# Performance work log

Measured on AMD Instinct MI355X. Metric: run time of the kernel, lower is better.

The kernel has to match this reference:

```python
import jax, jax.numpy as jnp
import numpy as np

N, E, C, L = 50000, 625000, 128, 4
H = 2 * C  # hidden size of per-layer ObjectModel
FRAC_SCALE = 1.0 / 16.0   # fractional_bitwidth = 4
Q_MAX = 8.0               # int_bitwidth = 4 -> signed fixed point range [-8, 8 - 1/16]


def fq(x):
    """Fixed-point fake-quantize (4 int bits, 4 frac bits, signed)."""
    return jnp.clip(jnp.round(x / FRAC_SCALE) * FRAC_SCALE, -Q_MAX, Q_MAX - FRAC_SCALE)


def qlin(h, W, b):
    # QuantLinear: input/weight/bias/output all quantized
    return fq(fq(h) @ fq(W) + fq(b))


def qbn(h, w, b):
    # BatchNorm1dToQuantScaleBias in inference: per-channel scale + bias
    return fq(fq(h) * fq(w) + fq(b))


def setup_inputs() -> dict:
    key = jax.random.key(0)
    ks = jax.random.split(key, 24)
    d = {}
    d["x"] = jax.random.normal(ks[0], (N, 3), dtype=jnp.float32)
    d["edge_attr"] = jax.random.normal(ks[1], (E, 4), dtype=jnp.float32)
    d["edge_index"] = jax.random.randint(ks[2], (2, E), 0, N, dtype=jnp.int64)
    # encoders
    d["node_W"] = jax.random.normal(ks[3], (3, C), dtype=jnp.float32) * 0.4
    d["node_b"] = jax.random.normal(ks[4], (C,), dtype=jnp.float32) * 0.2
    d["edge_W"] = jax.random.normal(ks[5], (4, C), dtype=jnp.float32) * 0.4
    d["edge_b"] = jax.random.normal(ks[6], (C,), dtype=jnp.float32) * 0.2
    d["node_bn_w"] = 1.0 + 0.1 * jax.random.normal(ks[7], (C,), dtype=jnp.float32)
    d["node_bn_b"] = 0.1 * jax.random.normal(ks[8], (C,), dtype=jnp.float32)
    d["edge_bn_w"] = 1.0 + 0.1 * jax.random.normal(ks[9], (C,), dtype=jnp.float32)
    d["edge_bn_b"] = 0.1 * jax.random.normal(ks[10], (C,), dtype=jnp.float32)
    # per-layer ObjectModel params (stacked over L)
    d["W1"] = jax.random.normal(ks[11], (L, C, H), dtype=jnp.float32) * (0.5 / np.sqrt(C))
    d["b1"] = jax.random.normal(ks[12], (L, H), dtype=jnp.float32) * 0.1
    d["bn_w"] = 1.0 + 0.1 * jax.random.normal(ks[13], (L, H), dtype=jnp.float32)
    d["bn_b"] = 0.1 * jax.random.normal(ks[14], (L, H), dtype=jnp.float32)
    d["W2"] = jax.random.normal(ks[15], (L, H, C), dtype=jnp.float32) * (0.5 / np.sqrt(H))
    d["b2"] = jax.random.normal(ks[16], (L, C), dtype=jnp.float32) * 0.1
    d["fc_W"] = jax.random.normal(ks[17], (C, 1), dtype=jnp.float32) * (0.5 / np.sqrt(C))
    d["fc_b"] = jax.random.normal(ks[18], (1,), dtype=jnp.float32) * 0.1
    return d


def reference(x, edge_attr, edge_index, node_W, node_b, edge_W, edge_b,
              node_bn_w, node_bn_b, edge_bn_w, edge_bn_b,
              W1, b1, bn_w, bn_b, W2, b2, fc_W, fc_b):
    src = edge_index[0]  # x_j (source) under flow='source_to_target'
    tgt = edge_index[1]  # aggregation target i

    h = fq(qlin(x, node_W, node_b))            # node encoder [N, C]
    e = fq(qlin(edge_attr, edge_W, edge_b))    # edge encoder [E, C]
    h = qbn(h, node_bn_w, node_bn_b)
    e = qbn(e, edge_bn_w, edge_bn_b)

    for l in range(L):
        # message: quant(x_j) + quant(edge_attr), QuantReLU
        msg = fq(jax.nn.relu(fq(h[src]) + fq(e)))          # [E, C]
        agg = jax.ops.segment_sum(msg, tgt, num_segments=N)  # scatter-sum [N, C]
        u = fq(agg)
        # ObjectModel: QuantLinear -> ScaleBias BN -> QuantReLU -> QuantLinear, then QuantIdentity
        z = qlin(u, W1[l], b1[l])
        z = qbn(z, bn_w[l], bn_b[l])
        z = fq(jax.nn.relu(z))
        z = fq(qlin(z, W2[l], b2[l]))
        h = h + z                                           # residual

    pooled = jnp.mean(h, axis=0, keepdims=True)  # global_mean_pool, batch=None -> [1, C]
    out = qlin(fq(pooled), fc_W, fc_b)           # [1, 1]
    out = fq(jax.nn.sigmoid(fq(out)))            # QuantSigmoid
    return out.reshape(-1)                       # [1]
```

## Files before the change

### kernel.cpp

```cpp
#include <hip/hip_runtime.h>
#include <stdint.h>

#define NN 50000
#define EE 625000
#define EPAD (EE + 16)
#define CC 128
#define HH 256
#define LL 4
#define NPAD 50048
#define NBLK (NPAD/64)
#define R2 32

typedef __attribute__((ext_vector_type(4))) int   i32x4;

__device__ __forceinline__ float qbf(float x){
  return fminf(127.f, fmaxf(-128.f, rintf(x*16.f)));
}
__device__ __forceinline__ float rq16(float t){
  return fminf(127.f, fmaxf(-128.f, rintf(t*0.0625f)));
}

__global__ void k_qbig(const float* __restrict__ W1, const float* __restrict__ W2,
                       signed char* __restrict__ w1q8, signed char* __restrict__ w2q8){
  int i = blockIdx.x*256 + threadIdx.x;
  if (i >= LL*CC*HH) return;
  {
    float v = qbf(W1[i]);
    int l = i / (CC*HH); int r = i - l*CC*HH; int c = r / HH; int hh = r - c*HH;
    w1q8[((size_t)l*HH + hh)*CC + c] = (signed char)v;
  }
  {
    float v = qbf(W2[i]);
    int l = i / (HH*CC); int r = i - l*HH*CC; int hh = r / CC; int c = r - hh*CC;
    w2q8[((size_t)l*CC + c)*HH + hh] = (signed char)v;
  }
}

struct QS { const float* s; float* d; int n; float m; };
struct QSArgs { QS q[14]; };

__global__ void k_qsmall(QSArgs a){
  for (int r=0;r<14;++r){
    QS qs = a.q[r];
    for (int i = blockIdx.x*blockDim.x + threadIdx.x; i < qs.n; i += gridDim.x*blockDim.x)
      qs.d[i] = qs.m * qbf(qs.s[i]);
  }
}

__global__ __launch_bounds__(256) void k_node_enc(
    const float* __restrict__ x, const float* __restrict__ nW,
    const float* __restrict__ nb16, const float* __restrict__ bnw,
    const float* __restrict__ bnb16, short* __restrict__ h0,
    signed char* __restrict__ hq8){
  int idx = blockIdx.x*256 + threadIdx.x;
  int n = idx >> 7, c = idx & 127;
  float x0 = qbf(x[n*3]), x1 = qbf(x[n*3+1]), x2 = qbf(x[n*3+2]);
  float S = x0*nW[c] + x1*nW[CC+c] + x2*nW[2*CC+c];
  float v1 = rq16(S + nb16[c]);
  float v2 = rq16(v1*bnw[c] + bnb16[c]);
  h0[idx] = (short)v2;
  hq8[idx] = (signed char)v2;
}

__global__ void k_deg(const int* __restrict__ ei, int* __restrict__ deg){
  int e = blockIdx.x*256 + threadIdx.x;
  if (e < EE) atomicAdd(&deg[ei[EE + e]], 1);
}

__global__ __launch_bounds__(256) void k_scanA(const int* __restrict__ deg,
                                               int* __restrict__ offI,
                                               int* __restrict__ btot){
  __shared__ int sh[256];
  int t = threadIdx.x;
  int base = blockIdx.x*1024 + t*4;
  int v[4]; int s = 0;
  #pragma unroll
  for (int i=0;i<4;++i){ v[i] = (base+i < NN) ? deg[base+i] : 0; s += v[i]; }
  sh[t] = s; __syncthreads();
  for (int off=1; off<256; off<<=1){
    int xv = (t>=off) ? sh[t-off] : 0;
    __syncthreads();
    sh[t] += xv;
    __syncthreads();
  }
  int run = (t>0) ? sh[t-1] : 0;
  #pragma unroll
  for (int i=0;i<4;++i){ run += v[i]; if (base+i < NN) offI[base+i] = run; }
  if (t==255) btot[blockIdx.x] = sh[255];
}

__global__ void k_scanB(const int* __restrict__ btot, int* __restrict__ boff, int nblk){
  if (threadIdx.x==0 && blockIdx.x==0){
    int run = 0;
    for (int b=0;b<nblk;++b){ int v = btot[b]; boff[b] = run; run += v; }
  }
}

__global__ void k_scanC(const int* __restrict__ boff, const int* __restrict__ deg,
                        int* __restrict__ offI, int* __restrict__ cursor){
  int i = blockIdx.x*256 + threadIdx.x;
  if (i < NN){
    int v = offI[i] + boff[i>>10];
    offI[i] = v;
    cursor[i] = v - deg[i];
  }
}

__global__ void k_fill(const int* __restrict__ ei, const float* __restrict__ ea,
                       int* __restrict__ cursor, int2* __restrict__ adjq){
  int e = blockIdx.x*256 + threadIdx.x;
  if (e < EE){
    int tgt = ei[EE + e];
    int p = atomicAdd(&cursor[tgt], 1);
    float4 v = ((const float4*)ea)[e];
    int b0 = (int)qbf(v.x) & 0xff, b1 = (int)qbf(v.y) & 0xff;
    int b2 = (int)qbf(v.z) & 0xff, b3 = (int)qbf(v.w) & 0xff;
    adjq[p] = make_int2(ei[e] * CC, b0 | (b1<<8) | (b2<<16) | (b3<<24));
  }
}

template<int FIRST>
__global__ __launch_bounds__(256) void k_msg(
    const int* __restrict__ offI, const int* __restrict__ deg_,
    const int2* __restrict__ adjq, signed char* __restrict__ eq,
    const float* __restrict__ ewf, const float* __restrict__ eb16,
    const float* __restrict__ ebnw, const float* __restrict__ ebnb16,
    const signed char* __restrict__ hq8, signed char* __restrict__ uq){
  int n = blockIdx.x*4 + (threadIdx.x >> 6);
  int lane = threadIdx.x & 63;
  int c0 = lane*2;
  float w0a,w1a,w2a,w3a,eba,bwa,bba, w0b,w1b,w2b,w3b,ebb,bwb,bbb;
  if (FIRST){
    w0a=ewf[c0];   w1a=ewf[CC+c0];   w2a=ewf[2*CC+c0];   w3a=ewf[3*CC+c0];
    eba=eb16[c0];  bwa=ebnw[c0];     bba=ebnb16[c0];
    w0b=ewf[c0+1]; w1b=ewf[CC+c0+1]; w2b=ewf[2*CC+c0+1]; w3b=ewf[3*CC+c0+1];
    ebb=eb16[c0+1];bwb=ebnw[c0+1];   bbb=ebnb16[c0+1];
  }
  int end = offI[n];
  int start = end - deg_[n];
  int acc0 = 0, acc1 = 0;
  for (int base = start; base < end; base += 16){
    int rem = end - base;
    int2 a = adjq[base + min(lane, rem-1)];
    ushort hv[16], ev[16];
    int qk[16];
    #pragma unroll
    for (int j=0;j<16;++j){
      int soj = __builtin_amdgcn_readlane(a.x, j);
      hv[j] = *(const ushort*)(hq8 + soj + c0);
      if (FIRST) qk[j] = __builtin_amdgcn_readlane(a.y, j);
      else       ev[j] = *(const ushort*)(eq + (((size_t)(base+j)) << 7) + c0);
    }
    #pragma unroll
    for (int j=0;j<16;++j){
      if (j < rem){
        int h0 = ((int)hv[j] << 24) >> 24;
        int h1 = ((int)(short)hv[j]) >> 8;
        int e0, e1;
        if (FIRST){
          int q = qk[j];
          float qx = (float)(int)(signed char)(q & 0xff);
          float qy = (float)(int)(signed char)((q>>8) & 0xff);
          float qz = (float)(int)(signed char)((q>>16) & 0xff);
          float qw = (float)(int)(signed char)(q>>24);
          float Sa = qx*w0a + qy*w1a + qz*w2a + qw*w3a;
          float Sb = qx*w0b + qy*w1b + qz*w2b + qw*w3b;
          e0 = (int)rq16(rq16(Sa + eba)*bwa + bba);
          e1 = (int)rq16(rq16(Sb + ebb)*bwb + bbb);
          *(ushort*)(eq + (((size_t)(base+j)) << 7) + c0) =
              (ushort)((e0 & 0xff) | ((e1 & 0xff) << 8));
        } else {
          e0 = ((int)ev[j] << 24) >> 24;
          e1 = ((int)(short)ev[j]) >> 8;
        }
        acc0 += min(max(h0 + e0, 0), 127);
        acc1 += min(max(h1 + e1, 0), 127);
      }
    }
  }
  int ua = min(acc0, 127), ub = min(acc1, 127);
  *(ushort*)(uq + (size_t)n*CC + c0) = (ushort)((ua & 0xff) | ((ub & 0xff) << 8));
}

__global__ __launch_bounds__(256, 3) void k_om(
    int l, const signed char* __restrict__ uq,
    const signed char* __restrict__ w1q8, const float* __restrict__ b1q16,
    const float* __restrict__ bnwf, const float* __restrict__ bnb16,
    const signed char* __restrict__ w2q8, const float* __restrict__ b2q16,
    const short* __restrict__ h_in, short* __restrict__ h_out,
    signed char* __restrict__ hq8, int* __restrict__ partial){
  __shared__ signed char uL[64][144];
  __shared__ signed char zL[64][272];
  int t = threadIdx.x;
  int nb = blockIdx.x * 64;
  {
    const i32x4* src = (const i32x4*)(uq + (size_t)nb*CC + t*32);
    int flat = t*32; int r = flat >> 7, c = flat & 127;
    *(i32x4*)&uL[r][c]      = src[0];
    *(i32x4*)&uL[r][c + 16] = src[1];
  }
  int lane = t & 63, wv = t >> 6;
  int lr = lane & 15, lk = lane >> 4;
  const signed char* W1p = w1q8 + (size_t)l*HH*CC;
  i32x4 w1f[2][4];
  #pragma unroll
  for (int ks=0; ks<2; ++ks)
    #pragma unroll
    for (int ci=0; ci<4; ++ci)
      w1f[ks][ci] = *(const i32x4*)(W1p + (size_t)(wv*64 + ci*16 + lr)*CC + ks*64 + lk*16);
  __syncthreads();

  i32x4 acc[4][4];
  #pragma unroll
  for (int mi=0;mi<4;++mi)
    #pragma unroll
    for (int ci=0;ci<4;++ci) acc[mi][ci] = (i32x4){0,0,0,0};
  #pragma unroll
  for (int ks=0; ks<2; ++ks){
    i32x4 av[4];
    #pragma unroll
    for (int mi=0;mi<4;++mi) av[mi] = *(const i32x4*)&uL[mi*16+lr][ks*64 + lk*16];
    #pragma unroll
    for (int mi=0;mi<4;++mi)
      #pragma unroll
      for (int ci=0;ci<4;++ci)
        acc[mi][ci] = __builtin_amdgcn_mfma_i32_16x16x64_i8(av[mi], w1f[ks][ci], acc[mi][ci], 0,0,0);
  }
  #pragma unroll
  for (int ci=0;ci<4;++ci){
    int hcol = wv*64 + ci*16 + lr;
    float b1 = b1q16[l*HH + hcol];
    float bw = bnwf[l*HH + hcol];
    float bb = bnb16[l*HH + hcol];
    #pragma unroll
    for (int mi=0;mi<4;++mi){
      #pragma unroll
      for (int r=0;r<4;++r){
        float v1 = rq16((float)acc[mi][ci][r] + b1);
        float v2 = fmaxf(rq16(v1*bw + bb), 0.f);
        zL[mi*16 + lk*4 + r][hcol] = (signed char)v2;
      }
    }
  }
  const signed char* W2p = w2q8 + (size_t)l*CC*HH;
  i32x4 w2f[4][2];
  #pragma unroll
  for (int ks=0; ks<4; ++ks)
    #pragma unroll
    for (int ci=0; ci<2; ++ci)
      w2f[ks][ci] = *(const i32x4*)(W2p + (size_t)(wv*32 + ci*16 + lr)*HH + ks*64 + lk*16);
  __syncthreads();

  i32x4 a2[4][2];
  #pragma unroll
  for (int mi=0;mi<4;++mi){ a2[mi][0] = (i32x4){0,0,0,0}; a2[mi][1] = (i32x4){0,0,0,0}; }
  #pragma unroll
  for (int ks=0; ks<4; ++ks){
    i32x4 av[4];
    #pragma unroll
    for (int mi=0;mi<4;++mi) av[mi] = *(const i32x4*)&zL[mi*16+lr][ks*64 + lk*16];
    #pragma unroll
    for (int mi=0;mi<4;++mi)
      #pragma unroll
      for (int ci=0;ci<2;++ci)
        a2[mi][ci] = __builtin_amdgcn_mfma_i32_16x16x64_i8(av[mi], w2f[ks][ci], a2[mi][ci], 0,0,0);
  }
  int psum[2] = {0, 0};
  #pragma unroll
  for (int ci=0;ci<2;++ci){
    int ccol = wv*32 + ci*16 + lr;
    float b2 = b2q16[l*CC + ccol];
    #pragma unroll
    for (int mi=0;mi<4;++mi){
      #pragma unroll
      for (int r=0;r<4;++r){
        int node = nb + mi*16 + lk*4 + r;
        float v = rq16((float)a2[mi][ci][r] + b2);
        int hn = (int)h_in[(size_t)node*CC + ccol] + (int)v;
        if (node < NN){
          h_out[(size_t)node*CC + ccol] = (short)hn;
          hq8[(size_t)node*CC + ccol] = (signed char)min(max(hn, -128), 127);
          psum[ci] += hn;
        }
      }
    }
  }
  if (partial){
    #pragma unroll
    for (int ci=0;ci<2;++ci){
      int s = psum[ci];
      s += __shfl_xor(s, 16);
      s += __shfl_xor(s, 32);
      if (lk == 0)
        partial[blockIdx.x*CC + wv*32 + ci*16 + lr] = s;
    }
  }
}

__global__ __launch_bounds__(256) void k_red(
    const int* __restrict__ partial, int* __restrict__ partial2){
  int t = threadIdx.x;
  int c = t & 127;
  int sub = blockIdx.x*2 + (t >> 7);
  int s = 0;
  for (int b = sub; b < NBLK; b += R2) s += partial[b*CC + c];
  partial2[sub*CC + c] = s;
}

__global__ __launch_bounds__(256) void k_final(
    const int* __restrict__ partial2, const float* __restrict__ fcwf,
    const float* __restrict__ fcb16, float* __restrict__ out){
  __shared__ int ired[128];
  __shared__ float red[128];
  int t = threadIdx.x;
  int c = t & 127, half = t >> 7;
  int s = 0;
  #pragma unroll
  for (int b = half; b < R2; b += 2) s += partial2[b*CC + c];
  if (half) ired[c] = s;
  __syncthreads();
  if (!half){
    int sc = s + ired[c];
    double m = (double)sc / (double)NN;
    float pq = fminf(127.f, fmaxf(-128.f, (float)rint(m)));
    red[c] = pq * fcwf[c];
  }
  __syncthreads();
  for (int o=64;o>0;o>>=1){ if (t<o) red[t] += red[t+o]; __syncthreads(); }
  if (t==0){
    float v = rq16(red[0] + fcb16[0]);
    float o1 = v * 0.0625f;
    float sg = 1.f/(1.f + expf(-o1));
    float oq = fminf(127.f, fmaxf(-128.f, rintf(sg*16.f)));
    out[0] = oq * 0.0625f;
  }
}

extern "C" void kernel_launch(void* const* d_in, const int* in_sizes, int n_in,
                              void* d_out, int out_size, void* d_ws, size_t ws_size,
                              hipStream_t stream){
  (void)in_sizes; (void)n_in; (void)out_size; (void)ws_size;
  const float* x   = (const float*)d_in[0];
  const float* ea  = (const float*)d_in[1];
  const int*   ei  = (const int*)d_in[2];
  const float* W1  = (const float*)d_in[11];
  const float* W2  = (const float*)d_in[15];

  char* w = (char*)d_ws;
  auto alloc = [&](size_t bytes)->char*{
    char* p = w; w += (bytes + 255) & ~(size_t)255; return p;
  };
  short* h0        = (short*)alloc((size_t)NPAD*CC*2);
  short* h1        = (short*)alloc((size_t)NPAD*CC*2);
  signed char* hq8 = (signed char*)alloc((size_t)NPAD*CC);
  signed char* uq  = (signed char*)alloc((size_t)NPAD*CC);
  int2* adjq       = (int2*)alloc((size_t)EPAD*8);
  int* deg         = (int*)alloc(NN*4);
  int* offI        = (int*)alloc(NN*4);
  int* cursor      = (int*)alloc(NN*4);
  int* btot        = (int*)alloc(64*4);
  int* boff        = (int*)alloc(64*4);
  int* partial     = (int*)alloc((size_t)NBLK*CC*4);
  int* partial2    = (int*)alloc((size_t)R2*CC*4);
  signed char* w1q8= (signed char*)alloc((size_t)LL*CC*HH);
  signed char* w2q8= (signed char*)alloc((size_t)LL*CC*HH);
  float* nodeWf    = (float*)alloc(3*CC*4);
  float* nb16f     = (float*)alloc(CC*4);
  float* nbnwf     = (float*)alloc(CC*4);
  float* nbnb16f   = (float*)alloc(CC*4);
  float* ewf       = (float*)alloc(4*CC*4);
  float* eb16f     = (float*)alloc(CC*4);
  float* ebnwf     = (float*)alloc(CC*4);
  float* ebnb16f   = (float*)alloc(CC*4);
  float* b1q16f    = (float*)alloc(LL*HH*4);
  float* bnwf      = (float*)alloc(LL*HH*4);
  float* bnb16f    = (float*)alloc(LL*HH*4);
  float* b2q16f    = (float*)alloc(LL*CC*4);
  float* fcwf      = (float*)alloc(CC*4);
  float* fcb16f    = (float*)alloc(256);
  signed char* eq  = (signed char*)alloc((size_t)EPAD*CC);

  hipMemsetAsync(deg, 0, NN*4, stream);

  k_qbig<<<(LL*CC*HH + 255)/256, 256, 0, stream>>>(W1, W2, w1q8, w2q8);

  QSArgs qa;
  auto setq = [&](int r, int idx, float* d, int n, float m){
    qa.q[r].s = (const float*)d_in[idx]; qa.q[r].d = d; qa.q[r].n = n; qa.q[r].m = m;
  };
  setq(0, 3,  nodeWf,  3*CC, 1.f);
  setq(1, 4,  nb16f,   CC,   16.f);
  setq(2, 5,  ewf,     4*CC, 1.f);
  setq(3, 6,  eb16f,   CC,   16.f);
  setq(4, 7,  nbnwf,   CC,   1.f);
  setq(5, 8,  nbnb16f, CC,   16.f);
  setq(6, 9,  ebnwf,   CC,   1.f);
  setq(7, 10, ebnb16f, CC,   16.f);
  setq(8, 12, b1q16f,  LL*HH, 16.f);
  setq(9, 13, bnwf,    LL*HH, 1.f);
  setq(10,14, bnb16f,  LL*HH, 16.f);
  setq(11,16, b2q16f,  LL*CC, 16.f);
  setq(12,17, fcwf,    CC,   1.f);
  setq(13,18, fcb16f,  1,    16.f);
  k_qsmall<<<4, 256, 0, stream>>>(qa);

  k_node_enc<<<(NN*CC)/256, 256, 0, stream>>>(x, nodeWf, nb16f, nbnwf, nbnb16f, h0, hq8);
  k_deg<<<(EE+255)/256, 256, 0, stream>>>(ei, deg);
  int nblk = (NN + 1023)/1024;
  k_scanA<<<nblk, 256, 0, stream>>>(deg, offI, btot);
  k_scanB<<<1, 64, 0, stream>>>(btot, boff, nblk);
  k_scanC<<<(NN+255)/256, 256, 0, stream>>>(boff, deg, offI, cursor);
  k_fill<<<(EE+255)/256, 256, 0, stream>>>(ei, ea, cursor, adjq);

  for (int l=0;l<LL;++l){
    const short* hi = (l & 1) ? h1 : h0;
    short* ho       = (l & 1) ? h0 : h1;
    if (l == 0)
      k_msg<1><<<NN/4, 256, 0, stream>>>(offI, deg, adjq, eq,
                                         ewf, eb16f, ebnwf, ebnb16f, hq8, uq);
    else
      k_msg<0><<<NN/4, 256, 0, stream>>>(offI, deg, adjq, eq,
                                         ewf, eb16f, ebnwf, ebnb16f, hq8, uq);
    k_om<<<NBLK, 256, 0, stream>>>(l, uq, w1q8, b1q16f, bnwf, bnb16f,
                                   w2q8, b2q16f, hi, ho, hq8,
                                   (l == LL-1) ? partial : nullptr);
  }
  k_red<<<R2/2, 256, 0, stream>>>(partial, partial2);
  k_final<<<1, 256, 0, stream>>>(partial2, fcwf, fcb16f, (float*)d_out);
}
```

Before: 360.5 us.

## Recompute edge encoding per layer with integer dot4 instead of storing eq

Removes the materialized 80MB per-edge encoded feature buffer eq, which was written in layer 0 and read back in layers 1-3. Each message pass now recomputes the edge encoder from the packed 4-byte quantized edge attributes using integer sdot4 and integer round-half-even requantization. A small init kernel packs the edge weights and biases into an int4 per channel. This trades heavy memory traffic for a few extra integer ALU ops per edge per layer, and relies on the integer arithmetic reproducing the float rounding exactly.

```diff
diff --git a/kernel.cpp b/kernel.cpp
--- a/kernel.cpp
+++ b/kernel.cpp
@@ -19,6 +19,22 @@
 __device__ __forceinline__ float rq16(float t){
   return fminf(127.f, fmaxf(-128.f, rintf(t*0.0625f)));
 }
+__device__ __forceinline__ int rne16c(int t){
+  int q = (t + 7 + ((t>>4)&1)) >> 4;
+  return min(max(q, -128), 127);
+}
+__device__ __forceinline__ int dot4b(int q, int w, int c){
+#if __has_builtin(__builtin_amdgcn_sdot4)
+  return __builtin_amdgcn_sdot4(q, w, c, false);
+#else
+  int s = c;
+  #pragma unroll
+  for (int i=0;i<4;++i)
+    s += ((int)(signed char)((q >> (8*i)) & 0xff)) *
+         ((int)(signed char)((w >> (8*i)) & 0xff));
+  return s;
+#endif
+}
 
 __global__ void k_qbig(const float* __restrict__ W1, const float* __restrict__ W2,
                        signed char* __restrict__ w1q8, signed char* __restrict__ w2q8){
@@ -37,14 +53,28 @@
 }
 
 struct QS { const float* s; float* d; int n; float m; };
-struct QSArgs { QS q[14]; };
+struct QSArgs { QS q[10]; };
 
 __global__ void k_qsmall(QSArgs a){
-  for (int r=0;r<14;++r){
+  for (int r=0;r<10;++r){
     QS qs = a.q[r];
     for (int i = blockIdx.x*blockDim.x + threadIdx.x; i < qs.n; i += gridDim.x*blockDim.x)
       qs.d[i] = qs.m * qbf(qs.s[i]);
   }
+}
+
+__global__ void k_epki(const float* __restrict__ eW, const float* __restrict__ eb,
+                       const float* __restrict__ bnw, const float* __restrict__ bnb,
+                       int4* __restrict__ epk){
+  int c = threadIdx.x;
+  int w0 = (int)qbf(eW[c])      & 0xff;
+  int w1 = (int)qbf(eW[CC+c])   & 0xff;
+  int w2 = (int)qbf(eW[2*CC+c]) & 0xff;
+  int w3 = (int)qbf(eW[3*CC+c]) & 0xff;
+  epk[c] = make_int4(w0 | (w1<<8) | (w2<<16) | (w3<<24),
+                     16 * (int)qbf(eb[c]),
+                     (int)qbf(bnw[c]),
+                     16 * (int)qbf(bnb[c]));
 }
 
 __global__ __launch_bounds__(256) void k_node_enc(
@@ -119,60 +149,38 @@
   }
 }
 
-template<int FIRST>
 __global__ __launch_bounds__(256) void k_msg(
     const int* __restrict__ offI, const int* __restrict__ deg_,
-    const int2* __restrict__ adjq, signed char* __restrict__ eq,
-    const float* __restrict__ ewf, const float* __restrict__ eb16,
-    const float* __restrict__ ebnw, const float* __restrict__ ebnb16,
+    const int2* __restrict__ adjq, const int4* __restrict__ epk,
     const signed char* __restrict__ hq8, signed char* __restrict__ uq){
   int n = blockIdx.x*4 + (threadIdx.x >> 6);
   int lane = threadIdx.x & 63;
   int c0 = lane*2;
-  float w0a,w1a,w2a,w3a,eba,bwa,bba, w0b,w1b,w2b,w3b,ebb,bwb,bbb;
-  if (FIRST){
-    w0a=ewf[c0];   w1a=ewf[CC+c0];   w2a=ewf[2*CC+c0];   w3a=ewf[3*CC+c0];
-    eba=eb16[c0];  bwa=ebnw[c0];     bba=ebnb16[c0];
-    w0b=ewf[c0+1]; w1b=ewf[CC+c0+1]; w2b=ewf[2*CC+c0+1]; w3b=ewf[3*CC+c0+1];
-    ebb=eb16[c0+1];bwb=ebnw[c0+1];   bbb=ebnb16[c0+1];
-  }
+  int4 P0 = epk[c0];
+  int4 P1 = epk[c0+1];
   int end = offI[n];
   int start = end - deg_[n];
   int acc0 = 0, acc1 = 0;
   for (int base = start; base < end; base += 16){
     int rem = end - base;
     int2 a = adjq[base + min(lane, rem-1)];
-    ushort hv[16], ev[16];
-    int qk[16];
+    ushort hv[16]; int qk[16];
     #pragma unroll
     for (int j=0;j<16;++j){
       int soj = __builtin_amdgcn_readlane(a.x, j);
       hv[j] = *(const ushort*)(hq8 + soj + c0);
-      if (FIRST) qk[j] = __builtin_amdgcn_readlane(a.y, j);
-      else       ev[j] = *(const ushort*)(eq + (((size_t)(base+j)) << 7) + c0);
+      qk[j] = __builtin_amdgcn_readlane(a.y, j);
     }
     #pragma unroll
     for (int j=0;j<16;++j){
       if (j < rem){
         int h0 = ((int)hv[j] << 24) >> 24;
         int h1 = ((int)(short)hv[j]) >> 8;
-        int e0, e1;
-        if (FIRST){
-          int q = qk[j];
-          float qx = (float)(int)(signed char)(q & 0xff);
-          float qy = (float)(int)(signed char)((q>>8) & 0xff);
-          float qz = (float)(int)(signed char)((q>>16) & 0xff);
-          float qw = (float)(int)(signed char)(q>>24);
-          float Sa = qx*w0a + qy*w1a + qz*w2a + qw*w3a;
-          float Sb = qx*w0b + qy*w1b + qz*w2b + qw*w3b;
-          e0 = (int)rq16(rq16(Sa + eba)*bwa + bba);
-          e1 = (int)rq16(rq16(Sb + ebb)*bwb + bbb);
-          *(ushort*)(eq + (((size_t)(base+j)) << 7) + c0) =
-              (ushort)((e0 & 0xff) | ((e1 & 0xff) << 8));
-        } else {
-          e0 = ((int)ev[j] << 24) >> 24;
-          e1 = ((int)(short)ev[j]) >> 8;
-        }
+        int q = qk[j];
+        int v10 = rne16c(dot4b(q, P0.x, P0.y));
+        int v11 = rne16c(dot4b(q, P1.x, P1.y));
+        int e0 = rne16c(v10*P0.z + P0.w);
+        int e1 = rne16c(v11*P1.z + P1.w);
         acc0 += min(max(h0 + e0, 0), 127);
         acc1 += min(max(h1 + e1, 0), 127);
       }
@@ -368,17 +376,13 @@
   float* nb16f     = (float*)alloc(CC*4);
   float* nbnwf     = (float*)alloc(CC*4);
   float* nbnb16f   = (float*)alloc(CC*4);
-  float* ewf       = (float*)alloc(4*CC*4);
-  float* eb16f     = (float*)alloc(CC*4);
-  float* ebnwf     = (float*)alloc(CC*4);
-  float* ebnb16f   = (float*)alloc(CC*4);
   float* b1q16f    = (float*)alloc(LL*HH*4);
   float* bnwf      = (float*)alloc(LL*HH*4);
   float* bnb16f    = (float*)alloc(LL*HH*4);
   float* b2q16f    = (float*)alloc(LL*CC*4);
   float* fcwf      = (float*)alloc(CC*4);
   float* fcb16f    = (float*)alloc(256);
-  signed char* eq  = (signed char*)alloc((size_t)EPAD*CC);
+  int4* epk        = (int4*)alloc(CC*16);
 
   hipMemsetAsync(deg, 0, NN*4, stream);
 
@@ -390,19 +394,17 @@
   };
   setq(0, 3,  nodeWf,  3*CC, 1.f);
   setq(1, 4,  nb16f,   CC,   16.f);
-  setq(2, 5,  ewf,     4*CC, 1.f);
-  setq(3, 6,  eb16f,   CC,   16.f);
-  setq(4, 7,  nbnwf,   CC,   1.f);
-  setq(5, 8,  nbnb16f, CC,   16.f);
-  setq(6, 9,  ebnwf,   CC,   1.f);
-  setq(7, 10, ebnb16f, CC,   16.f);
-  setq(8, 12, b1q16f,  LL*HH, 16.f);
-  setq(9, 13, bnwf,    LL*HH, 1.f);
-  setq(10,14, bnb16f,  LL*HH, 16.f);
-  setq(11,16, b2q16f,  LL*CC, 16.f);
-  setq(12,17, fcwf,    CC,   1.f);
-  setq(13,18, fcb16f,  1,    16.f);
+  setq(2, 7,  nbnwf,   CC,   1.f);
+  setq(3, 8,  nbnb16f, CC,   16.f);
+  setq(4, 12, b1q16f,  LL*HH, 16.f);
+  setq(5, 13, bnwf,    LL*HH, 1.f);
+  setq(6, 14, bnb16f,  LL*HH, 16.f);
+  setq(7, 16, b2q16f,  LL*CC, 16.f);
+  setq(8, 17, fcwf,    CC,   1.f);
+  setq(9, 18, fcb16f,  1,    16.f);
   k_qsmall<<<4, 256, 0, stream>>>(qa);
+  k_epki<<<1, 128, 0, stream>>>((const float*)d_in[5], (const float*)d_in[6],
+                                (const float*)d_in[9], (const float*)d_in[10], epk);
 
   k_node_enc<<<(NN*CC)/256, 256, 0, stream>>>(x, nodeWf, nb16f, nbnwf, nbnb16f, h0, hq8);
   k_deg<<<(EE+255)/256, 256, 0, stream>>>(ei, deg);
@@ -415,12 +417,7 @@
   for (int l=0;l<LL;++l){
     const short* hi = (l & 1) ? h1 : h0;
     short* ho       = (l & 1) ? h0 : h1;
-    if (l == 0)
-      k_msg<1><<<NN/4, 256, 0, stream>>>(offI, deg, adjq, eq,
-                                         ewf, eb16f, ebnwf, ebnb16f, hq8, uq);
-    else
-      k_msg<0><<<NN/4, 256, 0, stream>>>(offI, deg, adjq, eq,
-                                         ewf, eb16f, ebnwf, ebnb16f, hq8, uq);
+    k_msg<<<NN/4, 256, 0, stream>>>(offI, deg, adjq, epk, hq8, uq);
     k_om<<<NBLK, 256, 0, stream>>>(l, uq, w1q8, b1q16f, bnwf, bnb16f,
                                    w2q8, b2q16f, hi, ho, hq8,
                                    (l == LL-1) ? partial : nullptr);
```

After: 380.3 us. 5.5% more time.
